# Kernel tuning notes

Measured on AMD Instinct MI355X. Metric: run time of the kernel, lower is better.

Reference implementation:

```python
import jax, jax.numpy as jnp
import numpy as np

CPS = 16          # coarse_patch_size = 128 / resolution[0](=8)
ENC = 128         # enc_dim = CPS*CPS/2
LN_EPS = 1e-5


def setup_inputs() -> dict:
    key = jax.random.key(0)
    ks = jax.random.split(key, 10)
    B, C, H, W = 4, 256, 160, 160
    s = 0.05
    return {
        "feat_c1": jax.random.normal(ks[0], (B, C, H, W), dtype=jnp.float32),
        "feat_c2": jax.random.normal(ks[1], (B, C, H, W), dtype=jnp.float32),
        "mask_c1": jnp.ones((1, H, W), dtype=bool),
        "img_conv_w": jax.random.normal(ks[2], (1, C), dtype=jnp.float32) * s,
        "img_conv_b": jnp.zeros((1,), jnp.float32),
        "img_w1": jax.random.normal(ks[3], (2 * ENC, 2 * ENC), dtype=jnp.float32) * s,
        "img_w2": jax.random.normal(ks[4], (ENC, 2 * ENC), dtype=jnp.float32) * s,
        "img_ln_g": jnp.ones((ENC,), jnp.float32),
        "img_ln_b": jnp.zeros((ENC,), jnp.float32),
        "depth_conv_w": jax.random.normal(ks[5], (1, C), dtype=jnp.float32) * s,
        "depth_conv_b": jnp.zeros((1,), jnp.float32),
        "depth_w1": jax.random.normal(ks[6], (2 * ENC, 2 * ENC), dtype=jnp.float32) * s,
        "depth_w2": jax.random.normal(ks[7], (ENC, 2 * ENC), dtype=jnp.float32) * s,
        "depth_ln_g": jnp.ones((ENC,), jnp.float32),
        "depth_ln_b": jnp.zeros((ENC,), jnp.float32),
        "logit_scale": jnp.asarray(np.log(1.0 / 0.07), jnp.float32),
    }


def _grid_from_mask(mask_c1):
    # replicate get_patches: grid size from max lit row/col of the mask
    m = np.asarray(mask_c1)[0]
    inds = np.argwhere(m)
    feat_h = int(inds[:, 0].max()) + 1
    feat_w = int(inds[:, 1].max()) + 1
    nv = int(feat_w / CPS + 0.5)   # outer loop count (row starts), as in source
    nh = int(feat_h / CPS + 0.5)   # inner loop count (col starts)
    return nv, nh


def _extract_patches(feat, nv, nh):
    # vectorized equivalent of the nested python-loop gather: non-overlapping
    # CPS x CPS tiles, row-major order matching (r outer, c inner)
    B, C = feat.shape[0], feat.shape[1]
    f = feat[:, :, : nv * CPS, : nh * CPS]
    f = f.reshape(B, C, nv, CPS, nh, CPS)
    f = f.transpose(0, 2, 4, 1, 3, 5)          # [B, nv, nh, C, CPS, CPS]
    return f.reshape(B * nv * nh, C, CPS, CPS)


def _branch(patches, conv_w, conv_b, w1, w2, ln_g, ln_b):
    # conv1x1 (256 -> 1) + ReLU
    x = jnp.einsum("bchw,oc->bohw", patches, conv_w) + conv_b[None, :, None, None]
    x = jax.nn.relu(x)
    x = x.reshape(x.shape[0], -1)              # [B*N, 2*ENC]
    # Linear(no bias) -> ReLU -> Linear(no bias)
    x = jax.nn.relu(x @ w1.T) @ w2.T           # [B*N, ENC]
    mu = jnp.mean(x, axis=-1, keepdims=True)
    var = jnp.var(x, axis=-1, keepdims=True)
    return (x - mu) / jnp.sqrt(var + LN_EPS) * ln_g + ln_b


def reference(feat_c1, feat_c2, mask_c1, img_conv_w, img_conv_b, img_w1, img_w2,
              img_ln_g, img_ln_b, depth_conv_w, depth_conv_b, depth_w1, depth_w2,
              depth_ln_g, depth_ln_b, logit_scale):
    nv, nh = _grid_from_mask(mask_c1)
    N = nv * nh
    B = feat_c1.shape[0]
    p1 = _extract_patches(feat_c1, nv, nh)
    p2 = _extract_patches(feat_c2, nv, nh)
    e1 = _branch(p1, img_conv_w, img_conv_b, img_w1, img_w2, img_ln_g, img_ln_b)
    e2 = _branch(p2, depth_conv_w, depth_conv_b, depth_w1, depth_w2, depth_ln_g, depth_ln_b)
    e1 = e1.reshape(B, N, ENC)
    e2 = e2.reshape(B, N, ENC)
    scale = jnp.exp(logit_scale)
    logits_per_img = scale * jnp.einsum("bnd,bmd->bnm", e1, e2)   # [B, N, N]
    logits_per_depth = jnp.swapaxes(logits_per_img, 1, 2)
    return logits_per_img, logits_per_depth
```

## Files before the change

### kernel.cpp

```cpp
#include <hip/hip_runtime.h>
#include <math.h>

#define CPS 16
#define ENC 128
#define NH 10
#define NPATCH 100
#define BATCH 4
#define CCH 256
#define WIDTH 160
#define HW 25600
#define ROWS_TOTAL 400

__global__ __launch_bounds__(256) void conv_partial_kernel(
    const float* __restrict__ f1, const float* __restrict__ f2,
    const float* __restrict__ wci, const float* __restrict__ wcd,
    float* __restrict__ partial)
{
    int lane = threadIdx.x & 63;
    int wv   = threadIdx.x >> 6;

    int bid   = blockIdx.x;
    int cg    = bid & 15;
    int rest  = bid >> 4;
    int plane = rest & 7;
    int pxc   = rest >> 3;
    int branch = plane >> 2;
    int b      = plane & 3;

    const float* f    = branch ? f2  : f1;
    const float* wsel = branch ? wcd : wci;
    int c0 = cg * 16;

    int pxbase = pxc * 5120 + wv * 1280 + lane * 4;
    const float* fb = f + ((size_t)(b * CCH + c0)) * HW + pxbase;

    float4 acc[5] = {};
    #pragma unroll 4
    for (int c = 0; c < 16; ++c) {
        float wc = wsel[c0 + c];
        const float* p = fb + (size_t)c * HW;
        #pragma unroll
        for (int j = 0; j < 5; ++j) {
            float4 v = *(const float4*)(p + j * 256);
            acc[j].x = fmaf(v.x, wc, acc[j].x);
            acc[j].y = fmaf(v.y, wc, acc[j].y);
            acc[j].z = fmaf(v.z, wc, acc[j].z);
            acc[j].w = fmaf(v.w, wc, acc[j].w);
        }
    }

    float* pp = partial + (size_t)plane * HW + pxbase;
    #pragma unroll
    for (int j = 0; j < 5; ++j) {
        atomicAdd(pp + j * 256 + 0, acc[j].x);
        atomicAdd(pp + j * 256 + 1, acc[j].y);
        atomicAdd(pp + j * 256 + 2, acc[j].z);
        atomicAdd(pp + j * 256 + 3, acc[j].w);
    }
}

__global__ __launch_bounds__(256) void mlp_ln_kernel(
    const float* __restrict__ partial,
    const float* __restrict__ bci,  const float* __restrict__ bcd,
    const float* __restrict__ w1i, const float* __restrict__ w2i,
    const float* __restrict__ gi,  const float* __restrict__ bli,
    const float* __restrict__ w1d, const float* __restrict__ w2d,
    const float* __restrict__ gd,  const float* __restrict__ bld,
    float* __restrict__ e)
{
    const int R = 4;
    __shared__ float xs[R][256];
    __shared__ float ys[R][256];
    __shared__ float zs[R][ENC];

    int tid    = threadIdx.x;
    int branch = blockIdx.x / 100;
    int row0   = (blockIdx.x % 100) * R;

    const float* w1 = branch ? w1d : w1i;
    const float* w2 = branch ? w2d : w2i;
    const float* g  = branch ? gd  : gi;
    const float* bl = branch ? bld : bli;
    float bias      = branch ? bcd[0] : bci[0];

    {
        int hh = tid >> 4, ww = tid & 15;
        #pragma unroll
        for (int r = 0; r < R; ++r) {
            int prow  = row0 + r;
            int b     = prow / 100;
            int patch = prow % 100;
            int pv = patch / 10, ph = patch % 10;
            int pixel = (pv * 16 + hh) * WIDTH + ph * 16 + ww;
            float v = partial[(size_t)(branch * BATCH + b) * HW + pixel] + bias;
            xs[r][tid] = fmaxf(v, 0.f);
        }
    }
    __syncthreads();

    {
        float acc[R] = {0.f, 0.f, 0.f, 0.f};
        const float4* w1r = (const float4*)(w1 + (size_t)tid * 256);
        #pragma unroll 4
        for (int c4 = 0; c4 < 64; ++c4) {
            float4 wv = w1r[c4];
            #pragma unroll
            for (int r = 0; r < R; ++r) {
                float4 xv = *(const float4*)(&xs[r][c4 * 4]);
                acc[r] = fmaf(xv.x, wv.x, acc[r]);
                acc[r] = fmaf(xv.y, wv.y, acc[r]);
                acc[r] = fmaf(xv.z, wv.z, acc[r]);
                acc[r] = fmaf(xv.w, wv.w, acc[r]);
            }
        }
        #pragma unroll
        for (int r = 0; r < R; ++r) ys[r][tid] = fmaxf(acc[r], 0.f);
    }
    __syncthreads();

    #pragma unroll
    for (int i = 0; i < 2; ++i) {
        int idx = tid + 256 * i;
        int r = idx >> 7, m = idx & 127;
        float acc = 0.f;
        const float4* w2r = (const float4*)(w2 + (size_t)m * 256);
        #pragma unroll 4
        for (int c4 = 0; c4 < 64; ++c4) {
            float4 wv = w2r[c4];
            float4 yv = *(const float4*)(&ys[r][c4 * 4]);
            acc = fmaf(yv.x, wv.x, acc);
            acc = fmaf(yv.y, wv.y, acc);
            acc = fmaf(yv.z, wv.z, acc);
            acc = fmaf(yv.w, wv.w, acc);
        }
        zs[r][m] = acc;
    }
    __syncthreads();

    int r = tid >> 6, lane = tid & 63;
    float a  = zs[r][lane];
    float b2 = zs[r][lane + 64];
    float s = a + b2;
    float q = a * a + b2 * b2;
    #pragma unroll
    for (int off = 32; off >= 1; off >>= 1) {
        s += __shfl_xor(s, off);
        q += __shfl_xor(q, off);
    }
    float mu  = s * (1.f / 128.f);
    float var = q * (1.f / 128.f) - mu * mu;
    float inv = 1.f / sqrtf(var + 1e-5f);
    float* erow = e + ((size_t)(branch * ROWS_TOTAL + row0 + r)) * ENC;
    erow[lane]      = (a  - mu) * inv * g[lane]      + bl[lane];
    erow[lane + 64] = (b2 - mu) * inv * g[lane + 64] + bl[lane + 64];
}

__global__ __launch_bounds__(256) void logits_kernel(
    const float* __restrict__ e, const float* __restrict__ lsc,
    float* __restrict__ out)
{
    int gidx = blockIdx.x * 256 + threadIdx.x;
    if (gidx >= BATCH * NPATCH * NPATCH) return;
    float scale = expf(lsc[0]);

    int b    = gidx / (NPATCH * NPATCH);
    int rrem = gidx % (NPATCH * NPATCH);
    int n = rrem / NPATCH, m = rrem % NPATCH;

    const float4* e1 = (const float4*)(e + (size_t)(b * NPATCH + n) * ENC);
    const float4* e2 = (const float4*)(e + (size_t)(ROWS_TOTAL + b * NPATCH + m) * ENC);
    float acc = 0.f;
    #pragma unroll 8
    for (int c4 = 0; c4 < ENC / 4; ++c4) {
        float4 av = e1[c4], bv = e2[c4];
        acc = fmaf(av.x, bv.x, acc);
        acc = fmaf(av.y, bv.y, acc);
        acc = fmaf(av.z, bv.z, acc);
        acc = fmaf(av.w, bv.w, acc);
    }
    float L = scale * acc;
    out[gidx] = L;
    out[BATCH * NPATCH * NPATCH + b * NPATCH * NPATCH + m * NPATCH + n] = L;
}

extern "C" void kernel_launch(void* const* d_in, const int* in_sizes, int n_in,
                              void* d_out, int out_size, void* d_ws, size_t ws_size,
                              hipStream_t stream) {
    const float* f1  = (const float*)d_in[0];
    const float* f2  = (const float*)d_in[1];
    const float* wci = (const float*)d_in[3];
    const float* bci = (const float*)d_in[4];
    const float* w1i = (const float*)d_in[5];
    const float* w2i = (const float*)d_in[6];
    const float* gi  = (const float*)d_in[7];
    const float* bli = (const float*)d_in[8];
    const float* wcd = (const float*)d_in[9];
    const float* bcd = (const float*)d_in[10];
    const float* w1d = (const float*)d_in[11];
    const float* w2d = (const float*)d_in[12];
    const float* gd  = (const float*)d_in[13];
    const float* bld = (const float*)d_in[14];
    const float* lsc = (const float*)d_in[15];

    float* partial = (float*)d_ws;
    float* e       = partial + 2 * BATCH * HW;
    float* out = (float*)d_out;

    hipMemsetAsync(partial, 0, (size_t)2 * BATCH * HW * sizeof(float), stream);

    conv_partial_kernel<<<640, 256, 0, stream>>>(f1, f2, wci, wcd, partial);
    mlp_ln_kernel<<<200, 256, 0, stream>>>(partial, bci, bcd,
                                           w1i, w2i, gi, bli,
                                           w1d, w2d, gd, bld, e);
    logits_kernel<<<(BATCH * NPATCH * NPATCH + 255) / 256, 256, 0, stream>>>(e, lsc, out);
}
```

Measured before the change: 315.8 us.

## Replace atomic conv reduction with split-K partial buffers reduced in MLP kernel

```diff
diff --git a/kernel.cpp b/kernel.cpp
--- a/kernel.cpp
+++ b/kernel.cpp
@@ -10,8 +10,10 @@
 #define WIDTH 160
 #define HW 25600
 #define ROWS_TOTAL 400
-
-__global__ __launch_bounds__(256) void conv_partial_kernel(
+#define CSPLIT 8
+#define CHPG 32
+
+__global__ __launch_bounds__(256, 4) void conv_partial_kernel(
     const float* __restrict__ f1, const float* __restrict__ f2,
     const float* __restrict__ wci, const float* __restrict__ wcd,
     float* __restrict__ partial)
@@ -20,43 +22,36 @@
     int wv   = threadIdx.x >> 6;
 
     int bid   = blockIdx.x;
-    int cg    = bid & 15;
-    int rest  = bid >> 4;
-    int plane = rest & 7;
-    int pxc   = rest >> 3;
+    int plane = bid & 7;
+    int split = (bid >> 3) & 7;
+    int chunk = bid >> 6;
     int branch = plane >> 2;
     int b      = plane & 3;
 
     const float* f    = branch ? f2  : f1;
-    const float* wsel = branch ? wcd : wci;
-    int c0 = cg * 16;
-
-    int pxbase = pxc * 5120 + wv * 1280 + lane * 4;
-    const float* fb = f + ((size_t)(b * CCH + c0)) * HW + pxbase;
-
-    float4 acc[5] = {};
-    #pragma unroll 4
-    for (int c = 0; c < 16; ++c) {
-        float wc = wsel[c0 + c];
-        const float* p = fb + (size_t)c * HW;
-        #pragma unroll
-        for (int j = 0; j < 5; ++j) {
-            float4 v = *(const float4*)(p + j * 256);
-            acc[j].x = fmaf(v.x, wc, acc[j].x);
-            acc[j].y = fmaf(v.y, wc, acc[j].y);
-            acc[j].z = fmaf(v.z, wc, acc[j].z);
-            acc[j].w = fmaf(v.w, wc, acc[j].w);
-        }
-    }
-
-    float* pp = partial + (size_t)plane * HW + pxbase;
+    const float* wsel = (branch ? wcd : wci) + split * CHPG;
+
+    int px = chunk * 1024 + wv * 256 + lane * 4;
+    const float* fb = f + ((size_t)(b * CCH + split * CHPG)) * HW + px;
+
+    float4 acc = make_float4(0.f, 0.f, 0.f, 0.f);
     #pragma unroll
-    for (int j = 0; j < 5; ++j) {
-        atomicAdd(pp + j * 256 + 0, acc[j].x);
-        atomicAdd(pp + j * 256 + 1, acc[j].y);
-        atomicAdd(pp + j * 256 + 2, acc[j].z);
-        atomicAdd(pp + j * 256 + 3, acc[j].w);
-    }
+    for (int h = 0; h < 2; ++h) {
+        float4 v[16];
+        #pragma unroll
+        for (int j = 0; j < 16; ++j)
+            v[j] = *(const float4*)(fb + (size_t)(h * 16 + j) * HW);
+        #pragma unroll
+        for (int j = 0; j < 16; ++j) {
+            float wc = wsel[h * 16 + j];
+            acc.x = fmaf(v[j].x, wc, acc.x);
+            acc.y = fmaf(v[j].y, wc, acc.y);
+            acc.z = fmaf(v[j].z, wc, acc.z);
+            acc.w = fmaf(v[j].w, wc, acc.w);
+        }
+    }
+
+    *(float4*)(partial + ((size_t)(split * 8 + plane)) * HW + px) = acc;
 }
 
 __global__ __launch_bounds__(256) void mlp_ln_kernel(
@@ -92,7 +87,11 @@
             int patch = prow % 100;
             int pv = patch / 10, ph = patch % 10;
             int pixel = (pv * 16 + hh) * WIDTH + ph * 16 + ww;
-            float v = partial[(size_t)(branch * BATCH + b) * HW + pixel] + bias;
+            int plane = branch * BATCH + b;
+            float v = bias;
+            #pragma unroll
+            for (int s = 0; s < CSPLIT; ++s)
+                v += partial[((size_t)(s * 8 + plane)) * HW + pixel];
             xs[r][tid] = fmaxf(v, 0.f);
         }
     }
@@ -203,12 +202,10 @@
     const float* lsc = (const float*)d_in[15];
 
     float* partial = (float*)d_ws;
-    float* e       = partial + 2 * BATCH * HW;
+    float* e       = partial + CSPLIT * 8 * HW;
     float* out = (float*)d_out;
 
-    hipMemsetAsync(partial, 0, (size_t)2 * BATCH * HW * sizeof(float), stream);
-
-    conv_partial_kernel<<<640, 256, 0, stream>>>(f1, f2, wci, wcd, partial);
+    conv_partial_kernel<<<1600, 256, 0, stream>>>(f1, f2, wci, wcd, partial);
     mlp_ln_kernel<<<200, 256, 0, stream>>>(partial, bci, bcd,
                                            w1i, w2i, gi, bli,
                                            w1d, w2d, gd, bld, e);
```

Result: faster. 291.1 us (-7.8%).
